# Kernel optimization log

Hardware: AMD Instinct MI355X
Metric: run time of the kernel (lower is better)

The kernel has to match this reference:

```python
import jax, jax.numpy as jnp
import numpy as np

N_NODES = 100000


def gcn_conv(x, W, b, src, dst, ew, n):
    # PyG GCNConv with add_self_loops=True, symmetric normalization.
    # deg[i] = sum of incoming edge weights at i + 1.0 (self-loop weight 1)
    deg = jax.ops.segment_sum(ew, dst, num_segments=n) + 1.0
    dinv = jax.lax.rsqrt(deg)
    norm = dinv[src] * ew * dinv[dst]          # [E]
    h = x @ W                                  # [N, out]  (lin has no bias)
    msg = h[src] * norm[:, None]               # [E, out] gather + scale
    out = jax.ops.segment_sum(msg, dst, num_segments=n)
    out = out + h * (dinv * dinv)[:, None]     # self-loop contribution
    return out + b


def setup_inputs() -> dict:
    key = jax.random.key(0)
    ks = jax.random.split(key, 12)
    n, f = N_NODES, 128
    e = 1600000

    def lin_init(k, fin, fout):
        s = 1.0 / np.sqrt(fin)
        return jax.random.uniform(k, (fin, fout), jnp.float32, -s, s)

    return {
        "x": jax.random.normal(ks[0], (n, f), jnp.float32),
        "edge_index": jax.random.randint(ks[1], (2, e), 0, n, jnp.int64),
        "edge_attr": jax.random.uniform(ks[2], (e,), jnp.float32),
        "W1": lin_init(ks[3], f, 64),   "b1": jnp.zeros((64,), jnp.float32),
        "W2": lin_init(ks[4], 64, 128), "b2": jnp.zeros((128,), jnp.float32),
        "W3": lin_init(ks[5], 128, 256),"b3": jnp.zeros((256,), jnp.float32),
        "Wl1": lin_init(ks[6], 256, 128),
        "bl1": jax.random.uniform(ks[7], (128,), jnp.float32, -1/16.0, 1/16.0),
        "Wl2": lin_init(ks[8], 128, 10),
        "bl2": jax.random.uniform(ks[9], (10,), jnp.float32, -1/np.sqrt(128), 1/np.sqrt(128)),
    }


def reference(x, edge_index, edge_attr, W1, b1, W2, b2, W3, b3, Wl1, bl1, Wl2, bl2):
    src, dst = edge_index[0], edge_index[1]
    n = x.shape[0]
    h = jax.nn.relu(gcn_conv(x, W1, b1, src, dst, edge_attr, n))
    h = jax.nn.relu(gcn_conv(h, W2, b2, src, dst, edge_attr, n))
    h = jax.nn.relu(gcn_conv(h, W3, b3, src, dst, edge_attr, n))
    g = jnp.max(h, axis=0, keepdims=True)      # global_max_pool, batch=None -> [1, 256]
    g = jax.nn.relu(g @ Wl1 + bl1)
    # dropout p=0.5 is identity in eval mode
    logits = g @ Wl2 + bl2
    return jax.nn.log_softmax(logits, axis=1)
```

## Files before the change

kernel.cpp:

```cpp
#include <hip/hip_runtime.h>
#include <math.h>


typedef unsigned short u16;
typedef unsigned int   u32;
typedef unsigned long long u64;

typedef short bf16x8 __attribute__((ext_vector_type(8)));
typedef float f32x4  __attribute__((ext_vector_type(4)));

#define MAXR 64

__device__ __forceinline__ float bf2f(u16 u) {
    return __uint_as_float(((u32)u) << 16);
}
__device__ __forceinline__ u16 f2bf(float f) {
    u32 u = __float_as_uint(f);
    u32 r = (u + 0x7fffu + ((u >> 16) & 1u)) >> 16;
    return (u16)r;
}
__device__ __forceinline__ u32 pack2(float lo, float hi) {
    return (u32)f2bf(lo) | ((u32)f2bf(hi) << 16);
}


__global__ void deg_rank_scatter_kernel(const int* __restrict__ ei, const float* __restrict__ ew,
                                        u64* __restrict__ pk, uint2* __restrict__ edge2,
                                        int n, int E) {
    int e = blockIdx.x * blockDim.x + threadIdx.x;
    if (e < E) {
        int d = ei[E + e];
        int s = ei[e];
        float w = ew[e];
        u64 add = (1ULL << 48) | (u64)((double)w * 4294967296.0);
        u64 old = atomicAdd(&pk[(size_t)d * 8], add);
        int r = (int)(old >> 48);
        if (r < MAXR) edge2[(size_t)r * n + d] = make_uint2((u32)s, __float_as_uint(w));
    }
}

__global__ void finish_deg_kernel(const u64* __restrict__ pk, float* __restrict__ dinv, int n) {
    int i = blockIdx.x * blockDim.x + threadIdx.x;
    if (i < n) {
        double deg = (double)(pk[(size_t)i * 8] & ((1ULL << 48) - 1)) * (1.0 / 4294967296.0);
        dinv[i] = rsqrtf((float)deg + 1.0f);
    }
}

__global__ void cast_scale_kernel(const float* __restrict__ x, const float* __restrict__ dinv,
                                  u16* __restrict__ xs, int n) {
    int idx = blockIdx.x * blockDim.x + threadIdx.x;
    int node = idx >> 4, c = idx & 15;
    if (node < n) {
        float di = dinv[node];
        const float4* p = reinterpret_cast<const float4*>(&x[(size_t)node * 128 + c * 8]);
        float4 a = p[0], b = p[1];
        uint4 o;
        o.x = pack2(di * a.x, di * a.y);
        o.y = pack2(di * a.z, di * a.w);
        o.z = pack2(di * b.x, di * b.y);
        o.w = pack2(di * b.z, di * b.w);
        *reinterpret_cast<uint4*>(&xs[(size_t)node * 128 + c * 8]) = o;
    }
}

template<int FIN, int FOUT>
__global__ void wconv_kernel(const float* __restrict__ W, u16* __restrict__ Wf) {
    int t = blockIdx.x;
    int s = blockIdx.y;
    int l = threadIdx.x;
    int col = t * 16 + (l & 15);
    int k0 = s * 32 + 8 * (l >> 4);
    u32 packed[4];
    for (int jj = 0; jj < 4; ++jj) {
        u16 lo = f2bf(W[(size_t)(k0 + 2 * jj) * FOUT + col]);
        u16 hi = f2bf(W[(size_t)(k0 + 2 * jj + 1) * FOUT + col]);
        packed[jj] = (u32)lo | ((u32)hi << 16);
    }
    u32* dst = (u32*)&Wf[(((size_t)t * (FIN / 32) + s) * 64 + l) * 8];
    dst[0] = packed[0]; dst[1] = packed[1]; dst[2] = packed[2]; dst[3] = packed[3];
}

template<int F>
__global__ __launch_bounds__(256)
void agg_kernel(const u16* __restrict__ R, const u64* __restrict__ pk,
                const uint2* __restrict__ edge2,
                const float* __restrict__ dinv, u16* __restrict__ Z, int n) {
    constexpr int TPN = F / 8;
    constexpr int NPB = 256 / TPN;
    int t = threadIdx.x;
    int node = blockIdx.x * NPB + t / TPN;
    if (node >= n) return;
    int j8 = (t % TPN) * 8;
    int cnt = (int)(pk[(size_t)node * 8] >> 48);
    if (cnt > MAXR) cnt = MAXR;
    float di = dinv[node];

    uint4 sv = *reinterpret_cast<const uint4*>(&R[(size_t)node * F + j8]);
    float acc0, acc1, acc2, acc3, acc4, acc5, acc6, acc7;
    acc0 = bf2f((u16)sv.x);  acc1 = bf2f((u16)(sv.x >> 16));
    acc2 = bf2f((u16)sv.y);  acc3 = bf2f((u16)(sv.y >> 16));
    acc4 = bf2f((u16)sv.z);  acc5 = bf2f((u16)(sv.z >> 16));
    acc6 = bf2f((u16)sv.w);  acc7 = bf2f((u16)(sv.w >> 16));

    const uint2* ecol = edge2 + node;
    int e = 0;
    for (; e + 4 <= cnt; e += 4) {
        uint2 ed0 = ecol[(size_t)e * n];
        uint2 ed1 = ecol[(size_t)(e + 1) * n];
        uint2 ed2 = ecol[(size_t)(e + 2) * n];
        uint2 ed3 = ecol[(size_t)(e + 3) * n];
        uint4 h0 = *reinterpret_cast<const uint4*>(&R[(size_t)ed0.x * F + j8]);
        uint4 h1 = *reinterpret_cast<const uint4*>(&R[(size_t)ed1.x * F + j8]);
        uint4 h2 = *reinterpret_cast<const uint4*>(&R[(size_t)ed2.x * F + j8]);
        uint4 h3 = *reinterpret_cast<const uint4*>(&R[(size_t)ed3.x * F + j8]);
        float w0 = __uint_as_float(ed0.y);
        float w1 = __uint_as_float(ed1.y);
        float w2 = __uint_as_float(ed2.y);
        float w3 = __uint_as_float(ed3.y);
        acc0 += w0 * bf2f((u16)h0.x) + w1 * bf2f((u16)h1.x) + w2 * bf2f((u16)h2.x) + w3 * bf2f((u16)h3.x);
        acc1 += w0 * bf2f((u16)(h0.x >> 16)) + w1 * bf2f((u16)(h1.x >> 16)) + w2 * bf2f((u16)(h2.x >> 16)) + w3 * bf2f((u16)(h3.x >> 16));
        acc2 += w0 * bf2f((u16)h0.y) + w1 * bf2f((u16)h1.y) + w2 * bf2f((u16)h2.y) + w3 * bf2f((u16)h3.y);
        acc3 += w0 * bf2f((u16)(h0.y >> 16)) + w1 * bf2f((u16)(h1.y >> 16)) + w2 * bf2f((u16)(h2.y >> 16)) + w3 * bf2f((u16)(h3.y >> 16));
        acc4 += w0 * bf2f((u16)h0.z) + w1 * bf2f((u16)h1.z) + w2 * bf2f((u16)h2.z) + w3 * bf2f((u16)h3.z);
        acc5 += w0 * bf2f((u16)(h0.z >> 16)) + w1 * bf2f((u16)(h1.z >> 16)) + w2 * bf2f((u16)(h2.z >> 16)) + w3 * bf2f((u16)(h3.z >> 16));
        acc6 += w0 * bf2f((u16)h0.w) + w1 * bf2f((u16)h1.w) + w2 * bf2f((u16)h2.w) + w3 * bf2f((u16)h3.w);
        acc7 += w0 * bf2f((u16)(h0.w >> 16)) + w1 * bf2f((u16)(h1.w >> 16)) + w2 * bf2f((u16)(h2.w >> 16)) + w3 * bf2f((u16)(h3.w >> 16));
    }
    for (; e < cnt; ++e) {
        uint2 ed = ecol[(size_t)e * n];
        float w = __uint_as_float(ed.y);
        uint4 hv = *reinterpret_cast<const uint4*>(&R[(size_t)ed.x * F + j8]);
        acc0 += w * bf2f((u16)hv.x);  acc1 += w * bf2f((u16)(hv.x >> 16));
        acc2 += w * bf2f((u16)hv.y);  acc3 += w * bf2f((u16)(hv.y >> 16));
        acc4 += w * bf2f((u16)hv.z);  acc5 += w * bf2f((u16)(hv.z >> 16));
        acc6 += w * bf2f((u16)hv.w);  acc7 += w * bf2f((u16)(hv.w >> 16));
    }

    uint4 o;
    o.x = pack2(di * acc0, di * acc1);
    o.y = pack2(di * acc2, di * acc3);
    o.z = pack2(di * acc4, di * acc5);
    o.w = pack2(di * acc6, di * acc7);
    *reinterpret_cast<uint4*>(&Z[(size_t)node * F + j8]) = o;
}

template<int FIN, int FOUT, bool FUSE_MAX, bool SCALE_OUT>
__global__ __launch_bounds__(256)
void gemm_kernel(const u16* __restrict__ Zin, const u16* __restrict__ Wf,
                 const float* __restrict__ b, const float* __restrict__ dinv,
                 u16* __restrict__ Rout, float* __restrict__ g, int n) {
    constexpr int KS = FIN / 32;
    constexpr int NT = FOUT / 16;
    constexpr int Q8 = FIN / 8;
    __shared__ u16 Asw[4][KS][64][8];
    __shared__ int gsm[256];
    int tid = threadIdx.x;
    int gbase = blockIdx.x * 64;

    if (FUSE_MAX) gsm[tid] = 0;

    for (int idx = tid; idx < 64 * Q8; idx += 256) {
        int m = idx / Q8, q = idx - m * Q8;
        int gn = gbase + m;
        uint4 v = make_uint4(0, 0, 0, 0);
        if (gn < n) v = *reinterpret_cast<const uint4*>(&Zin[(size_t)gn * FIN + q * 8]);
        uint4* dst = reinterpret_cast<uint4*>(&Asw[m >> 4][q >> 2][((q & 3) << 4) | (m & 15)][0]);
        *dst = v;
    }
    __syncthreads();

    int w = tid >> 6, lane = tid & 63;
    int nodeq = gbase + w * 16 + ((lane >> 4) << 2);

    bf16x8 a[KS];
    #pragma unroll
    for (int s = 0; s < KS; ++s)
        a[s] = *reinterpret_cast<const bf16x8*>(&Asw[w][s][lane][0]);

    float dv[4];
    if (SCALE_OUT) {
        #pragma unroll
        for (int r = 0; r < 4; ++r) {
            int node = nodeq + r;
            dv[r] = (node < n) ? dinv[node] : 0.f;
        }
    }

    int col0 = lane & 15;
    #pragma unroll
    for (int t = 0; t < NT; ++t) {
        f32x4 acc = {0.f, 0.f, 0.f, 0.f};
        #pragma unroll
        for (int s = 0; s < KS; ++s) {
            bf16x8 bf = *reinterpret_cast<const bf16x8*>(&Wf[(((size_t)t * KS + s) * 64 + lane) * 8]);
            acc = __builtin_amdgcn_mfma_f32_16x16x32_bf16(a[s], bf, acc, 0, 0, 0);
        }
        int col = t * 16 + col0;
        float bb = b[col];
        if (FUSE_MAX) {
            float ml = 0.0f;
            #pragma unroll
            for (int r = 0; r < 4; ++r) {
                int node = nodeq + r;
                float v = acc[r] + bb;
                if (node < n) ml = fmaxf(ml, v);
            }
            ml = fmaxf(ml, __shfl_xor(ml, 16));
            ml = fmaxf(ml, __shfl_xor(ml, 32));
            if ((lane >> 4) == 0) atomicMax(&gsm[col], __float_as_int(ml));
        } else {
            #pragma unroll
            for (int r = 0; r < 4; ++r) {
                int node = nodeq + r;
                if (node < n) {
                    float v = fmaxf(acc[r] + bb, 0.0f);
                    if (SCALE_OUT) v *= dv[r];
                    Rout[(size_t)node * FOUT + col] = f2bf(v);
                }
            }
        }
    }
    if (FUSE_MAX) {
        __syncthreads();
        atomicMax(&((int*)g)[tid], gsm[tid]);
    }
}


__global__ void head_kernel(const float* __restrict__ g, const float* __restrict__ Wl1,
                            const float* __restrict__ bl1, const float* __restrict__ Wl2,
                            const float* __restrict__ bl2, float* __restrict__ out) {
    __shared__ float gs[256];
    __shared__ float ys[128];
    __shared__ float ls[10];
    int t = threadIdx.x;
    gs[t] = g[t];
    __syncthreads();
    if (t < 128) {
        float acc = bl1[t];
        for (int k = 0; k < 256; ++k) acc += gs[k] * Wl1[k * 128 + t];
        ys[t] = fmaxf(acc, 0.0f);
    }
    __syncthreads();
    if (t < 10) {
        float acc = bl2[t];
        for (int j = 0; j < 128; ++j) acc += ys[j] * Wl2[j * 10 + t];
        ls[t] = acc;
    }
    __syncthreads();
    if (t == 0) {
        float m = ls[0];
        for (int c = 1; c < 10; ++c) m = fmaxf(m, ls[c]);
        float se = 0.0f;
        for (int c = 0; c < 10; ++c) se += expf(ls[c] - m);
        float lse = logf(se);
        for (int c = 0; c < 10; ++c) out[c] = ls[c] - m - lse;
    }
}


static inline int cdiv(int a, int b) { return (a + b - 1) / b; }

extern "C" void kernel_launch(void* const* d_in, const int* in_sizes, int n_in,
                              void* d_out, int out_size, void* d_ws, size_t ws_size,
                              hipStream_t stream) {
    const float* x   = (const float*)d_in[0];
    const int*   ei  = (const int*)d_in[1];
    const float* ew  = (const float*)d_in[2];
    const float* W1  = (const float*)d_in[3];
    const float* b1  = (const float*)d_in[4];
    const float* W2  = (const float*)d_in[5];
    const float* b2  = (const float*)d_in[6];
    const float* W3  = (const float*)d_in[7];
    const float* b3  = (const float*)d_in[8];
    const float* Wl1 = (const float*)d_in[9];
    const float* bl1 = (const float*)d_in[10];
    const float* Wl2 = (const float*)d_in[11];
    const float* bl2 = (const float*)d_in[12];

    const int n = in_sizes[0] / 128;
    const int E = in_sizes[1] / 2;

    char* p = (char*)d_ws;
    auto alloc = [&](size_t bytes) { char* q = p; p += (bytes + 255) & ~(size_t)255; return q; };
    u64*   pk    = (u64*)  alloc((size_t)n * 64);
    float* dinv  = (float*)alloc((size_t)n * 4);
    uint2* edge2 = (uint2*)alloc((size_t)MAXR * n * 8);
    u16*   xs    = (u16*)  alloc((size_t)n * 128 * 2);
    u16*   z1    = (u16*)  alloc((size_t)n * 128 * 2);
    u16*   r2    = (u16*)  alloc((size_t)n * 64 * 2);
    u16*   z2    = (u16*)  alloc((size_t)n * 64 * 2);
    u16*   r3    = (u16*)  alloc((size_t)n * 128 * 2);
    u16*   z3    = (u16*)  alloc((size_t)n * 128 * 2);
    u16*   W1f   = (u16*)  alloc((size_t)128 * 64 * 2);
    u16*   W2f   = (u16*)  alloc((size_t)64 * 128 * 2);
    u16*   W3f   = (u16*)  alloc((size_t)128 * 256 * 2);
    float* g     = (float*)alloc(256 * 4);

    hipMemsetAsync(pk, 0, (size_t)n * 64, stream);
    hipMemsetAsync(g,  0, 256 * 4, stream);

    int eb = cdiv(E, 256);
    deg_rank_scatter_kernel<<<eb, 256, 0, stream>>>(ei, ew, pk, edge2, n, E);
    finish_deg_kernel<<<cdiv(n, 256), 256, 0, stream>>>(pk, dinv, n);
    cast_scale_kernel<<<cdiv(n * 16, 256), 256, 0, stream>>>(x, dinv, xs, n);

    wconv_kernel<128, 64><<<dim3(64 / 16, 128 / 32), 64, 0, stream>>>(W1, W1f);
    wconv_kernel<64, 128><<<dim3(128 / 16, 64 / 32), 64, 0, stream>>>(W2, W2f);
    wconv_kernel<128, 256><<<dim3(256 / 16, 128 / 32), 64, 0, stream>>>(W3, W3f);

    agg_kernel<128><<<cdiv(n, 16), 256, 0, stream>>>(xs, pk, edge2, dinv, z1, n);
    gemm_kernel<128, 64, false, true><<<cdiv(n, 64), 256, 0, stream>>>(z1, W1f, b1, dinv, r2, nullptr, n);
    agg_kernel<64><<<cdiv(n, 32), 256, 0, stream>>>(r2, pk, edge2, dinv, z2, n);
    gemm_kernel<64, 128, false, true><<<cdiv(n, 64), 256, 0, stream>>>(z2, W2f, b2, dinv, r3, nullptr, n);
    agg_kernel<128><<<cdiv(n, 16), 256, 0, stream>>>(r3, pk, edge2, dinv, z3, n);
    gemm_kernel<128, 256, true, false><<<cdiv(n, 64), 256, 0, stream>>>(z3, W3f, b3, dinv, nullptr, g, n);

    head_kernel<<<1, 256, 0, stream>>>(g, Wl1, bl1, Wl2, bl2, (float*)d_out);
}
```

Baseline: 382.3 us.

## Fuse neighbor aggregation into GEMM kernels and split edge rank/scatter

Each GCN layer now gathers neighbor features directly into the GEMM's shared-memory A tile, so the intermediate aggregated buffers z1/z2/z3 are neither written to nor read back from global memory. This also removes three kernel launches. The edge preprocessing is split into a rank-computing atomic kernel and a separate scatter kernel that go through a u16 rank buffer. The cost is extra edge-array traffic, and each fused block now does the gather for 64 nodes before its MFMA stage, which lengthens that stage's latency chain and may reduce overlap.

```diff
diff --git a/kernel.cpp b/kernel.cpp
--- a/kernel.cpp
+++ b/kernel.cpp
@@ -24,18 +24,28 @@
 }
 
 
-__global__ void deg_rank_scatter_kernel(const int* __restrict__ ei, const float* __restrict__ ew,
-                                        u64* __restrict__ pk, uint2* __restrict__ edge2,
-                                        int n, int E) {
+__global__ void deg_rank_kernel(const int* __restrict__ ei, const float* __restrict__ ew,
+                                u64* __restrict__ pk, u16* __restrict__ rank, int E) {
     int e = blockIdx.x * blockDim.x + threadIdx.x;
     if (e < E) {
         int d = ei[E + e];
-        int s = ei[e];
-        float w = ew[e];
-        u64 add = (1ULL << 48) | (u64)((double)w * 4294967296.0);
+        u64 add = (1ULL << 48) | (u64)((double)ew[e] * 4294967296.0);
         u64 old = atomicAdd(&pk[(size_t)d * 8], add);
-        int r = (int)(old >> 48);
-        if (r < MAXR) edge2[(size_t)r * n + d] = make_uint2((u32)s, __float_as_uint(w));
+        u64 r = old >> 48;
+        rank[e] = (u16)(r > 65535 ? 65535 : r);
+    }
+}
+
+__global__ void scatter_kernel(const int* __restrict__ ei, const float* __restrict__ ew,
+                               const u16* __restrict__ rank, uint2* __restrict__ edge2,
+                               int n, int E) {
+    int e = blockIdx.x * blockDim.x + threadIdx.x;
+    if (e < E) {
+        int r = (int)rank[e];
+        if (r < MAXR) {
+            int s = ei[e], d = ei[E + e];
+            edge2[(size_t)r * n + d] = make_uint2((u32)s, __float_as_uint(ew[e]));
+        }
     }
 }
 
@@ -81,78 +91,17 @@
     dst[0] = packed[0]; dst[1] = packed[1]; dst[2] = packed[2]; dst[3] = packed[3];
 }
 
-template<int F>
-__global__ __launch_bounds__(256)
-void agg_kernel(const u16* __restrict__ R, const u64* __restrict__ pk,
-                const uint2* __restrict__ edge2,
-                const float* __restrict__ dinv, u16* __restrict__ Z, int n) {
-    constexpr int TPN = F / 8;
-    constexpr int NPB = 256 / TPN;
-    int t = threadIdx.x;
-    int node = blockIdx.x * NPB + t / TPN;
-    if (node >= n) return;
-    int j8 = (t % TPN) * 8;
-    int cnt = (int)(pk[(size_t)node * 8] >> 48);
-    if (cnt > MAXR) cnt = MAXR;
-    float di = dinv[node];
-
-    uint4 sv = *reinterpret_cast<const uint4*>(&R[(size_t)node * F + j8]);
-    float acc0, acc1, acc2, acc3, acc4, acc5, acc6, acc7;
-    acc0 = bf2f((u16)sv.x);  acc1 = bf2f((u16)(sv.x >> 16));
-    acc2 = bf2f((u16)sv.y);  acc3 = bf2f((u16)(sv.y >> 16));
-    acc4 = bf2f((u16)sv.z);  acc5 = bf2f((u16)(sv.z >> 16));
-    acc6 = bf2f((u16)sv.w);  acc7 = bf2f((u16)(sv.w >> 16));
-
-    const uint2* ecol = edge2 + node;
-    int e = 0;
-    for (; e + 4 <= cnt; e += 4) {
-        uint2 ed0 = ecol[(size_t)e * n];
-        uint2 ed1 = ecol[(size_t)(e + 1) * n];
-        uint2 ed2 = ecol[(size_t)(e + 2) * n];
-        uint2 ed3 = ecol[(size_t)(e + 3) * n];
-        uint4 h0 = *reinterpret_cast<const uint4*>(&R[(size_t)ed0.x * F + j8]);
-        uint4 h1 = *reinterpret_cast<const uint4*>(&R[(size_t)ed1.x * F + j8]);
-        uint4 h2 = *reinterpret_cast<const uint4*>(&R[(size_t)ed2.x * F + j8]);
-        uint4 h3 = *reinterpret_cast<const uint4*>(&R[(size_t)ed3.x * F + j8]);
-        float w0 = __uint_as_float(ed0.y);
-        float w1 = __uint_as_float(ed1.y);
-        float w2 = __uint_as_float(ed2.y);
-        float w3 = __uint_as_float(ed3.y);
-        acc0 += w0 * bf2f((u16)h0.x) + w1 * bf2f((u16)h1.x) + w2 * bf2f((u16)h2.x) + w3 * bf2f((u16)h3.x);
-        acc1 += w0 * bf2f((u16)(h0.x >> 16)) + w1 * bf2f((u16)(h1.x >> 16)) + w2 * bf2f((u16)(h2.x >> 16)) + w3 * bf2f((u16)(h3.x >> 16));
-        acc2 += w0 * bf2f((u16)h0.y) + w1 * bf2f((u16)h1.y) + w2 * bf2f((u16)h2.y) + w3 * bf2f((u16)h3.y);
-        acc3 += w0 * bf2f((u16)(h0.y >> 16)) + w1 * bf2f((u16)(h1.y >> 16)) + w2 * bf2f((u16)(h2.y >> 16)) + w3 * bf2f((u16)(h3.y >> 16));
-        acc4 += w0 * bf2f((u16)h0.z) + w1 * bf2f((u16)h1.z) + w2 * bf2f((u16)h2.z) + w3 * bf2f((u16)h3.z);
-        acc5 += w0 * bf2f((u16)(h0.z >> 16)) + w1 * bf2f((u16)(h1.z >> 16)) + w2 * bf2f((u16)(h2.z >> 16)) + w3 * bf2f((u16)(h3.z >> 16));
-        acc6 += w0 * bf2f((u16)h0.w) + w1 * bf2f((u16)h1.w) + w2 * bf2f((u16)h2.w) + w3 * bf2f((u16)h3.w);
-        acc7 += w0 * bf2f((u16)(h0.w >> 16)) + w1 * bf2f((u16)(h1.w >> 16)) + w2 * bf2f((u16)(h2.w >> 16)) + w3 * bf2f((u16)(h3.w >> 16));
-    }
-    for (; e < cnt; ++e) {
-        uint2 ed = ecol[(size_t)e * n];
-        float w = __uint_as_float(ed.y);
-        uint4 hv = *reinterpret_cast<const uint4*>(&R[(size_t)ed.x * F + j8]);
-        acc0 += w * bf2f((u16)hv.x);  acc1 += w * bf2f((u16)(hv.x >> 16));
-        acc2 += w * bf2f((u16)hv.y);  acc3 += w * bf2f((u16)(hv.y >> 16));
-        acc4 += w * bf2f((u16)hv.z);  acc5 += w * bf2f((u16)(hv.z >> 16));
-        acc6 += w * bf2f((u16)hv.w);  acc7 += w * bf2f((u16)(hv.w >> 16));
-    }
-
-    uint4 o;
-    o.x = pack2(di * acc0, di * acc1);
-    o.y = pack2(di * acc2, di * acc3);
-    o.z = pack2(di * acc4, di * acc5);
-    o.w = pack2(di * acc6, di * acc7);
-    *reinterpret_cast<uint4*>(&Z[(size_t)node * F + j8]) = o;
-}
-
 template<int FIN, int FOUT, bool FUSE_MAX, bool SCALE_OUT>
 __global__ __launch_bounds__(256)
-void gemm_kernel(const u16* __restrict__ Zin, const u16* __restrict__ Wf,
-                 const float* __restrict__ b, const float* __restrict__ dinv,
-                 u16* __restrict__ Rout, float* __restrict__ g, int n) {
-    constexpr int KS = FIN / 32;
-    constexpr int NT = FOUT / 16;
-    constexpr int Q8 = FIN / 8;
+void fused_layer_kernel(const u16* __restrict__ R, const u64* __restrict__ pk,
+                        const uint2* __restrict__ edge2, const float* __restrict__ dinv,
+                        const u16* __restrict__ Wf, const float* __restrict__ b,
+                        u16* __restrict__ Rout, float* __restrict__ g, int n) {
+    constexpr int KS  = FIN / 32;
+    constexpr int NT  = FOUT / 16;
+    constexpr int TPN = FIN / 8;
+    constexpr int NPB = 256 / TPN;
+    constexpr int NIT = 64 / NPB;
     __shared__ u16 Asw[4][KS][64][8];
     __shared__ int gsm[256];
     int tid = threadIdx.x;
@@ -160,13 +109,63 @@
 
     if (FUSE_MAX) gsm[tid] = 0;
 
-    for (int idx = tid; idx < 64 * Q8; idx += 256) {
-        int m = idx / Q8, q = idx - m * Q8;
-        int gn = gbase + m;
-        uint4 v = make_uint4(0, 0, 0, 0);
-        if (gn < n) v = *reinterpret_cast<const uint4*>(&Zin[(size_t)gn * FIN + q * 8]);
-        uint4* dst = reinterpret_cast<uint4*>(&Asw[m >> 4][q >> 2][((q & 3) << 4) | (m & 15)][0]);
-        *dst = v;
+    int sub = tid / TPN;
+    int q   = tid % TPN;
+    #pragma unroll
+    for (int it = 0; it < NIT; ++it) {
+        int m = it * NPB + sub;
+        int node = gbase + m;
+        float acc[8];
+        #pragma unroll
+        for (int j = 0; j < 8; ++j) acc[j] = 0.f;
+
+        if (node < n) {
+            int cnt = (int)(pk[(size_t)node * 8] >> 48);
+            if (cnt > MAXR) cnt = MAXR;
+            float di = dinv[node];
+
+            auto fmadd = [&](float w, uint4 h) {
+                acc[0] += w * bf2f((u16)h.x);  acc[1] += w * bf2f((u16)(h.x >> 16));
+                acc[2] += w * bf2f((u16)h.y);  acc[3] += w * bf2f((u16)(h.y >> 16));
+                acc[4] += w * bf2f((u16)h.z);  acc[5] += w * bf2f((u16)(h.z >> 16));
+                acc[6] += w * bf2f((u16)h.w);  acc[7] += w * bf2f((u16)(h.w >> 16));
+            };
+
+            uint4 sv = *reinterpret_cast<const uint4*>(&R[(size_t)node * FIN + q * 8]);
+            fmadd(1.0f, sv);
+
+            const uint2* ecol = edge2 + node;
+            int e = 0;
+            for (; e + 4 <= cnt; e += 4) {
+                uint2 ed0 = ecol[(size_t)e * n];
+                uint2 ed1 = ecol[(size_t)(e + 1) * n];
+                uint2 ed2 = ecol[(size_t)(e + 2) * n];
+                uint2 ed3 = ecol[(size_t)(e + 3) * n];
+                uint4 h0 = *reinterpret_cast<const uint4*>(&R[(size_t)ed0.x * FIN + q * 8]);
+                uint4 h1 = *reinterpret_cast<const uint4*>(&R[(size_t)ed1.x * FIN + q * 8]);
+                uint4 h2 = *reinterpret_cast<const uint4*>(&R[(size_t)ed2.x * FIN + q * 8]);
+                uint4 h3 = *reinterpret_cast<const uint4*>(&R[(size_t)ed3.x * FIN + q * 8]);
+                fmadd(__uint_as_float(ed0.y), h0);
+                fmadd(__uint_as_float(ed1.y), h1);
+                fmadd(__uint_as_float(ed2.y), h2);
+                fmadd(__uint_as_float(ed3.y), h3);
+            }
+            for (; e < cnt; ++e) {
+                uint2 ed = ecol[(size_t)e * n];
+                uint4 hv = *reinterpret_cast<const uint4*>(&R[(size_t)ed.x * FIN + q * 8]);
+                fmadd(__uint_as_float(ed.y), hv);
+            }
+
+            #pragma unroll
+            for (int j = 0; j < 8; ++j) acc[j] *= di;
+        }
+
+        uint4 o;
+        o.x = pack2(acc[0], acc[1]);
+        o.y = pack2(acc[2], acc[3]);
+        o.z = pack2(acc[4], acc[5]);
+        o.w = pack2(acc[6], acc[7]);
+        *reinterpret_cast<uint4*>(&Asw[m >> 4][q >> 2][((q & 3) << 4) | (m & 15)][0]) = o;
     }
     __syncthreads();
 
@@ -286,13 +285,11 @@
     auto alloc = [&](size_t bytes) { char* q = p; p += (bytes + 255) & ~(size_t)255; return q; };
     u64*   pk    = (u64*)  alloc((size_t)n * 64);
     float* dinv  = (float*)alloc((size_t)n * 4);
+    u16*   rank  = (u16*)  alloc((size_t)E * 2);
     uint2* edge2 = (uint2*)alloc((size_t)MAXR * n * 8);
     u16*   xs    = (u16*)  alloc((size_t)n * 128 * 2);
-    u16*   z1    = (u16*)  alloc((size_t)n * 128 * 2);
     u16*   r2    = (u16*)  alloc((size_t)n * 64 * 2);
-    u16*   z2    = (u16*)  alloc((size_t)n * 64 * 2);
     u16*   r3    = (u16*)  alloc((size_t)n * 128 * 2);
-    u16*   z3    = (u16*)  alloc((size_t)n * 128 * 2);
     u16*   W1f   = (u16*)  alloc((size_t)128 * 64 * 2);
     u16*   W2f   = (u16*)  alloc((size_t)64 * 128 * 2);
     u16*   W3f   = (u16*)  alloc((size_t)128 * 256 * 2);
@@ -302,7 +299,8 @@
     hipMemsetAsync(g,  0, 256 * 4, stream);
 
     int eb = cdiv(E, 256);
-    deg_rank_scatter_kernel<<<eb, 256, 0, stream>>>(ei, ew, pk, edge2, n, E);
+    deg_rank_kernel<<<eb, 256, 0, stream>>>(ei, ew, pk, rank, E);
+    scatter_kernel<<<eb, 256, 0, stream>>>(ei, ew, rank, edge2, n, E);
     finish_deg_kernel<<<cdiv(n, 256), 256, 0, stream>>>(pk, dinv, n);
     cast_scale_kernel<<<cdiv(n * 16, 256), 256, 0, stream>>>(x, dinv, xs, n);
 
@@ -310,12 +308,9 @@
     wconv_kernel<64, 128><<<dim3(128 / 16, 64 / 32), 64, 0, stream>>>(W2, W2f);
     wconv_kernel<128, 256><<<dim3(256 / 16, 128 / 32), 64, 0, stream>>>(W3, W3f);
 
-    agg_kernel<128><<<cdiv(n, 16), 256, 0, stream>>>(xs, pk, edge2, dinv, z1, n);
-    gemm_kernel<128, 64, false, true><<<cdiv(n, 64), 256, 0, stream>>>(z1, W1f, b1, dinv, r2, nullptr, n);
-    agg_kernel<64><<<cdiv(n, 32), 256, 0, stream>>>(r2, pk, edge2, dinv, z2, n);
-    gemm_kernel<64, 128, false, true><<<cdiv(n, 64), 256, 0, stream>>>(z2, W2f, b2, dinv, r3, nullptr, n);
-    agg_kernel<128><<<cdiv(n, 16), 256, 0, stream>>>(r3, pk, edge2, dinv, z3, n);
-    gemm_kernel<128, 256, true, false><<<cdiv(n, 64), 256, 0, stream>>>(z3, W3f, b3, dinv, nullptr, g, n);
+    fused_layer_kernel<128, 64, false, true><<<cdiv(n, 64), 256, 0, stream>>>(xs, pk, edge2, dinv, W1f, b1, r2, nullptr, n);
+    fused_layer_kernel<64, 128, false, true><<<cdiv(n, 64), 256, 0, stream>>>(r2, pk, edge2, dinv, W2f, b2, r3, nullptr, n);
+    fused_layer_kernel<128, 256, true, false><<<cdiv(n, 64), 256, 0, stream>>>(r3, pk, edge2, dinv, W3f, b3, nullptr, g, n);
 
     head_kernel<<<1, 256, 0, stream>>>(g, Wl1, bl1, Wl2, bl2, (float*)d_out);
 }
```

Result: faster. 347.1 us (-9.2%).
